# Kernel optimization log

Measured on AMD Instinct MI355X. Metric: run time of the kernel, lower is better.

## Reference

```python
import jax, jax.numpy as jnp
import numpy as np

B, S, H, V = 64, 512, 1024, 32000


def setup_inputs() -> dict:
    key = jax.random.key(0)
    ks = jax.random.split(key, 20)
    sd = 0.02
    inp = {
        'x': jax.random.randint(ks[0], (B, 1), 0, V),
        'h_prev': jax.random.normal(ks[1], (B, H), dtype=jnp.float32),
        'annotations': jax.random.normal(ks[2], (B, S, H), dtype=jnp.float32),
        # embedding table
        'emb': jax.random.normal(ks[3], (V, H), dtype=jnp.float32) * sd,
        # attention MLP: Linear(2H -> H), ReLU, Linear(H -> 1)
        'attn_W1': jax.random.normal(ks[4], (H, 2 * H), dtype=jnp.float32) * sd,
        'attn_b1': jnp.zeros((H,), jnp.float32),
        'attn_W2': jax.random.normal(ks[5], (1, H), dtype=jnp.float32) * sd,
        'attn_b2': jnp.zeros((1,), jnp.float32),
        # GRU cell linears (input_size = 2H). NOTE: original code has a bug where
        # weights_hr is never used (r uses weights_hz); we replicate that, so no Whr.
        'W_ir': jax.random.normal(ks[6], (H, 2 * H), dtype=jnp.float32) * sd,
        'b_ir': jnp.zeros((H,), jnp.float32),
        'W_iz': jax.random.normal(ks[7], (H, 2 * H), dtype=jnp.float32) * sd,
        'b_iz': jnp.zeros((H,), jnp.float32),
        'W_in': jax.random.normal(ks[8], (H, 2 * H), dtype=jnp.float32) * sd,
        'b_in': jnp.zeros((H,), jnp.float32),
        'W_hz': jax.random.normal(ks[9], (H, H), dtype=jnp.float32) * sd,
        'b_hz': jnp.zeros((H,), jnp.float32),
        'W_hn': jax.random.normal(ks[10], (H, H), dtype=jnp.float32) * sd,
        'b_hn': jnp.zeros((H,), jnp.float32),
        # output projection H -> V
        'W_out': jax.random.normal(ks[11], (V, H), dtype=jnp.float32) * sd,
        'b_out': jnp.zeros((V,), jnp.float32),
    }
    return inp


def _lin(x, W, b):
    # torch nn.Linear: y = x @ W.T + b, W has shape (out, in)
    return x @ W.T + b


def reference(x, h_prev, annotations, emb, attn_W1, attn_b1, attn_W2, attn_b2,
              W_ir, b_ir, W_iz, b_iz, W_in, b_in, W_hz, b_hz, W_hn, b_hn,
              W_out, b_out):
    # embedding lookup, squeeze time dim: (B, H)
    embed = emb[x[:, 0]]

    # additive attention: concat(annotations, expanded hidden) -> MLP -> softmax
    # split W1 over the concat axis to avoid materializing the [B,S,2H] concat:
    # concat @ W1.T == annotations @ W1[:, :H].T + hidden @ W1[:, H:].T
    hA = jnp.einsum('bsh,kh->bsk', annotations, attn_W1[:, :H])  # (B,S,H)
    hB = h_prev @ attn_W1[:, H:].T                               # (B,H)
    hidden_act = jax.nn.relu(hA + hB[:, None, :] + attn_b1)
    scores = jnp.einsum('bsk,k->bs', hidden_act, attn_W2[0]) + attn_b2[0]
    attention_weights = jax.nn.softmax(scores, axis=1)[:, :, None]  # (B,S,1)

    # context vector
    context = jnp.sum(attention_weights * annotations, axis=1)  # (B,H)
    xc = jnp.concatenate([context, embed], axis=1)              # (B,2H)

    # GRU cell (faithful to the original, including the weights_hz reuse in r)
    hz = _lin(h_prev, W_hz, b_hz)
    z = jax.nn.sigmoid(_lin(xc, W_iz, b_iz) + hz)
    r = jax.nn.sigmoid(_lin(xc, W_ir, b_ir) + hz)  # bug replicated: uses W_hz
    g = jnp.tanh(_lin(xc, W_in, b_in) + r * _lin(h_prev, W_hn, b_hn))
    h_new = (1.0 - z) * g + z * h_prev

    output = _lin(h_new, W_out, b_out)  # (B,V)
    return output, h_new, attention_weights
```

## Files before the change

### kernel.cpp

```cpp
#include <hip/hip_runtime.h>


typedef __bf16 bf16;
typedef __attribute__((ext_vector_type(4))) float  f32x4;
typedef __attribute__((ext_vector_type(4))) float  fx4;
typedef __attribute__((ext_vector_type(8))) bf16   bf16x8;
typedef __attribute__((ext_vector_type(4))) bf16   bf16x4;
typedef __attribute__((ext_vector_type(4))) unsigned int u32x4;
typedef __attribute__((ext_vector_type(2))) unsigned int u32x2;

#define MFMA16x16x32(a, b, c) __builtin_amdgcn_mfma_f32_16x16x32_bf16(a, b, c, 0, 0, 0)

#define Bb   64
#define Ss   512
#define Hh   1024
#define Vv   32000
#define Mtot (Bb * Ss)

#define WS_HNEW_B    131072
#define WS_XC_B      262144
#define WS_W1A_B     524288
#define WS_P_HB      2621440
#define WS_P_HZ      3670016
#define WS_P_HN      4718592
#define WS_P_IZ      5767168
#define WS_P_IR      6815744
#define WS_P_IN      7864320
#define WS_SCORES    8912896
#define WS_CTX       11010048
#define WS_ANNB      13107200

#define OUT_LOGITS   0
#define OUT_HNEW     2048000
#define OUT_AW       2113536

__device__ __forceinline__ float bf2f(unsigned short u) {
    unsigned int x = ((unsigned int)u) << 16;
    float f;
    __builtin_memcpy(&f, &x, 4);
    return f;
}

__device__ __forceinline__ void gload_lds16(const bf16* g, bf16* l)
{
    __builtin_amdgcn_global_load_lds(
        (const __attribute__((address_space(1))) unsigned int*)g,
        (__attribute__((address_space(3))) unsigned int*)l,
        16, 0, 0);
}

__global__ __launch_bounds__(256, 2) void k_pre(
    const int* __restrict__ x, const float* __restrict__ h_prev,
    const float* __restrict__ emb, const float* __restrict__ attn_W1,
    const float* __restrict__ W_hz, const float* __restrict__ W_hn,
    const float* __restrict__ ann,
    bf16* __restrict__ xc_b, bf16* __restrict__ W1a_b, bf16* __restrict__ annb,
    float* __restrict__ p_hB, float* __restrict__ p_hz, float* __restrict__ p_hn)
{
    __shared__ __align__(16) bf16 lA[2][64][72];
    __shared__ __align__(16) bf16 lB[2][64][72];

    int bid = blockIdx.x, t = threadIdx.x;

    if (bid >= 1280) {
        size_t i = ((size_t)(bid - 1280) * 256 + t) * 8;
        size_t stride = (size_t)2048 * 256 * 8;
        size_t n = (size_t)Mtot * Hh;
        for (; i < n; i += stride) {
            fx4 v0 = *(const fx4*)(ann + i);
            fx4 v1 = *(const fx4*)(ann + i + 4);
            bf16x8 o;
#pragma unroll
            for (int q = 0; q < 4; q++) { o[q] = (bf16)v0[q]; o[q + 4] = (bf16)v1[q]; }
            *(bf16x8*)(annb + i) = o;
        }
        return;
    }
    if (bid >= 192) {
        int sub = bid - 192;
        if (sub < 64) {
            int b = sub, row = x[b];
            for (int i = t; i < Hh; i += 256)
                xc_b[b * 2048 + Hh + i] = (bf16)emb[(size_t)row * Hh + i];
        } else {
            int row = sub - 64;
            int k4 = t * 4;
            fx4 v = *(const fx4*)(attn_W1 + (size_t)row * 2048 + k4);
            bf16x4 o;
#pragma unroll
            for (int q = 0; q < 4; q++) o[q] = (bf16)v[q];
            *(bf16x4*)(W1a_b + (size_t)row * Hh + k4) = o;
        }
        return;
    }

    int nb = bid & 15, sk = (bid >> 4) & 3, mat = bid >> 6;
    const float* Bp = (mat == 0) ? (attn_W1 + 1024) : (mat == 1 ? W_hz : W_hn);
    int ldb         = (mat == 0) ? 2048 : 1024;
    float* op       = (mat == 0) ? p_hB : (mat == 1 ? p_hz : p_hn);

    int n0 = nb * 64, k0 = sk * 256;
    int lane = t & 63, wid = t >> 6;
    int srow = t >> 2, schunk = t & 3;

    const float* agp = h_prev + (size_t)srow * 1024 + k0 + schunk * 16;
    const float* bgp = Bp + (size_t)(n0 + srow) * ldb + k0 + schunk * 16;

    f32x4 acc[4];
#pragma unroll
    for (int i = 0; i < 4; i++) acc[i] = (f32x4)0.0f;

    fx4 aRf[4], bRf[4];
#pragma unroll
    for (int q = 0; q < 4; q++) { aRf[q] = *(const fx4*)(agp + q * 4);
                                  bRf[q] = *(const fx4*)(bgp + q * 4); }
    {
        bf16x8 a0, a1, p0, p1;
#pragma unroll
        for (int q = 0; q < 4; q++) {
            a0[q] = (bf16)aRf[0][q]; a0[q + 4] = (bf16)aRf[1][q];
            a1[q] = (bf16)aRf[2][q]; a1[q + 4] = (bf16)aRf[3][q];
            p0[q] = (bf16)bRf[0][q]; p0[q + 4] = (bf16)bRf[1][q];
            p1[q] = (bf16)bRf[2][q]; p1[q + 4] = (bf16)bRf[3][q];
        }
        *(bf16x8*)&lA[0][srow][schunk * 16]     = a0;
        *(bf16x8*)&lA[0][srow][schunk * 16 + 8] = a1;
        *(bf16x8*)&lB[0][srow][schunk * 16]     = p0;
        *(bf16x8*)&lB[0][srow][schunk * 16 + 8] = p1;
    }
    __syncthreads();

    int cur = 0;
    for (int ks = 0; ks < 4; ks++) {
        if (ks + 1 < 4) {
#pragma unroll
            for (int q = 0; q < 4; q++) {
                aRf[q] = *(const fx4*)(agp + (ks + 1) * 64 + q * 4);
                bRf[q] = *(const fx4*)(bgp + (ks + 1) * 64 + q * 4);
            }
        }
        int rA = lane & 15;
        int kc = (lane >> 4) * 8;
#pragma unroll
        for (int kk = 0; kk < 2; kk++) {
            bf16x8 bfr = *(bf16x8*)&lB[cur][wid * 16 + rA][kk * 32 + kc];
#pragma unroll
            for (int i = 0; i < 4; i++) {
                bf16x8 af = *(bf16x8*)&lA[cur][i * 16 + rA][kk * 32 + kc];
                acc[i] = MFMA16x16x32(af, bfr, acc[i]);
            }
        }
        if (ks + 1 < 4) {
            int nxt = cur ^ 1;
            bf16x8 a0, a1, p0, p1;
#pragma unroll
            for (int q = 0; q < 4; q++) {
                a0[q] = (bf16)aRf[0][q]; a0[q + 4] = (bf16)aRf[1][q];
                a1[q] = (bf16)aRf[2][q]; a1[q + 4] = (bf16)aRf[3][q];
                p0[q] = (bf16)bRf[0][q]; p0[q + 4] = (bf16)bRf[1][q];
                p1[q] = (bf16)bRf[2][q]; p1[q + 4] = (bf16)bRf[3][q];
            }
            *(bf16x8*)&lA[nxt][srow][schunk * 16]     = a0;
            *(bf16x8*)&lA[nxt][srow][schunk * 16 + 8] = a1;
            *(bf16x8*)&lB[nxt][srow][schunk * 16]     = p0;
            *(bf16x8*)&lB[nxt][srow][schunk * 16 + 8] = p1;
        }
        __syncthreads();
        cur ^= 1;
    }

    int n = n0 + wid * 16 + (lane & 15);
#pragma unroll
    for (int i = 0; i < 4; i++)
#pragma unroll
        for (int r = 0; r < 4; r++) {
            int m = i * 16 + (lane >> 4) * 4 + r;
            op[(size_t)(sk * 64 + m) * 1024 + n] = acc[i][r];
        }
}

__global__ __launch_bounds__(256, 2) void k_sgemm(
    const bf16* __restrict__ A, int lda, int kchunk,
    const float* __restrict__ B0, const float* __restrict__ B1, const float* __restrict__ B2,
    int ldb0, int ldb1, int ldb2,
    float* __restrict__ o0, float* __restrict__ o1, float* __restrict__ o2,
    const float* __restrict__ bias, int N, int finalOut)
{
    __shared__ __align__(16) bf16 lA[2][64][72];
    __shared__ __align__(16) bf16 lB[2][64][72];

    int nb = blockIdx.x, sk = blockIdx.y, mat = blockIdx.z;
    const float* Bp = (mat == 0) ? B0 : (mat == 1 ? B1 : B2);
    int ldb         = (mat == 0) ? ldb0 : (mat == 1 ? ldb1 : ldb2);
    float* op       = (mat == 0) ? o0 : (mat == 1 ? o1 : o2);

    int n0 = nb * 64, k0 = sk * kchunk;
    int t = threadIdx.x, lane = t & 63, wid = t >> 6;
    int srow = t >> 2, schunk = t & 3;

    const bf16*  agp = A  + (size_t)srow * lda + k0 + schunk * 16;
    const float* bgp = Bp + (size_t)(n0 + srow) * ldb + k0 + schunk * 16;

    f32x4 acc[4];
#pragma unroll
    for (int i = 0; i < 4; i++) acc[i] = (f32x4)0.0f;

    u32x4 aR0, aR1; fx4 bRf[4];
    int nk = kchunk >> 6;

    aR0 = *(const u32x4*)(agp);
    aR1 = *(const u32x4*)(agp + 8);
#pragma unroll
    for (int q = 0; q < 4; q++) bRf[q] = *(const fx4*)(bgp + q * 4);
    {
        *(u32x4*)&lA[0][srow][schunk * 16]     = aR0;
        *(u32x4*)&lA[0][srow][schunk * 16 + 8] = aR1;
        bf16x8 p0, p1;
#pragma unroll
        for (int q = 0; q < 4; q++) {
            p0[q] = (bf16)bRf[0][q]; p0[q + 4] = (bf16)bRf[1][q];
            p1[q] = (bf16)bRf[2][q]; p1[q + 4] = (bf16)bRf[3][q];
        }
        *(bf16x8*)&lB[0][srow][schunk * 16]     = p0;
        *(bf16x8*)&lB[0][srow][schunk * 16 + 8] = p1;
    }
    __syncthreads();

    int cur = 0;
    for (int ks = 0; ks < nk; ks++) {
        if (ks + 1 < nk) {
            aR0 = *(const u32x4*)(agp + (ks + 1) * 64);
            aR1 = *(const u32x4*)(agp + (ks + 1) * 64 + 8);
#pragma unroll
            for (int q = 0; q < 4; q++) bRf[q] = *(const fx4*)(bgp + (ks + 1) * 64 + q * 4);
        }
        int rA = lane & 15;
        int kc = (lane >> 4) * 8;
#pragma unroll
        for (int kk = 0; kk < 2; kk++) {
            bf16x8 bfr = *(bf16x8*)&lB[cur][wid * 16 + rA][kk * 32 + kc];
#pragma unroll
            for (int i = 0; i < 4; i++) {
                bf16x8 af = *(bf16x8*)&lA[cur][i * 16 + rA][kk * 32 + kc];
                acc[i] = MFMA16x16x32(af, bfr, acc[i]);
            }
        }
        if (ks + 1 < nk) {
            int nxt = cur ^ 1;
            *(u32x4*)&lA[nxt][srow][schunk * 16]     = aR0;
            *(u32x4*)&lA[nxt][srow][schunk * 16 + 8] = aR1;
            bf16x8 p0, p1;
#pragma unroll
            for (int q = 0; q < 4; q++) {
                p0[q] = (bf16)bRf[0][q]; p0[q + 4] = (bf16)bRf[1][q];
                p1[q] = (bf16)bRf[2][q]; p1[q + 4] = (bf16)bRf[3][q];
            }
            *(bf16x8*)&lB[nxt][srow][schunk * 16]     = p0;
            *(bf16x8*)&lB[nxt][srow][schunk * 16 + 8] = p1;
        }
        __syncthreads();
        cur ^= 1;
    }

    int n = n0 + wid * 16 + (lane & 15);
#pragma unroll
    for (int i = 0; i < 4; i++) {
#pragma unroll
        for (int r = 0; r < 4; r++) {
            int m = i * 16 + (lane >> 4) * 4 + r;
            float v = acc[i][r];
            if (finalOut) op[(size_t)m * N + n] = v + bias[n];
            else          op[(size_t)(sk * 64 + m) * N + n] = v;
        }
    }
}

__global__ __launch_bounds__(512, 2) void k_attn(
    const bf16* __restrict__ annb, const bf16* __restrict__ Bw,
    const float* __restrict__ p_hB, const float* __restrict__ b1,
    const float* __restrict__ W2, float* __restrict__ scores_part)
{
    extern __shared__ char smem[];

    int bid = blockIdx.x;
    int wgid = (bid & 7) * 64 + (bid >> 3);
    int mb = wgid >> 2, nbp = wgid & 3;

    int t = threadIdx.x, lane = t & 63, wid = t >> 6;
    int wm = wid >> 2, wn = wid & 3;
    int r = lane & 15, q = lane >> 4;

    const bf16* aS = annb + (size_t)mb  * 262144
                   + (size_t)(wid * 32 + (lane >> 2)) * 1024 + (lane & 3) * 8;
    const bf16* bS = Bw   + (size_t)nbp * 262144
                   + (size_t)(wid * 32 + (lane >> 2)) * 1024 + (lane & 3) * 8;
    int sld = wid * 2048;

#define STAGE(kt) do { int bq_ = ((kt) & 3) * 32768;                         \
        const bf16* a_ = aS + (kt) * 32;                                     \
        const bf16* b_ = bS + (kt) * 32;                                     \
        gload_lds16(a_,         (bf16*)(smem + bq_ + sld));                  \
        gload_lds16(a_ + 16384, (bf16*)(smem + bq_ + sld + 1024));           \
        gload_lds16(b_,         (bf16*)(smem + bq_ + 16384 + sld));          \
        gload_lds16(b_ + 16384, (bf16*)(smem + bq_ + 16384 + sld + 1024));   \
    } while (0)

    int rAo[8], rBo[4];
#pragma unroll
    for (int i = 0; i < 8; i++)
        rAo[i] = (wm * 64 + (i & 3) * 16 + (i >> 2) * 128 + r) * 64 + q * 16;
#pragma unroll
    for (int j = 0; j < 4; j++)
        rBo[j] = 16384 + (wn * 32 + (j & 1) * 16 + (j >> 1) * 128 + r) * 64 + q * 16;

    f32x4 acc[8][4];
#pragma unroll
    for (int i = 0; i < 8; i++)
#pragma unroll
        for (int j = 0; j < 4; j++) acc[i][j] = (f32x4)0.0f;

    STAGE(0); STAGE(1); STAGE(2);
    asm volatile("s_waitcnt vmcnt(8)" ::: "memory");
    __builtin_amdgcn_s_barrier();

#pragma unroll 1
    for (int kt = 0; kt < 32; kt++) {
        const char* base = smem + (kt & 3) * 32768;
        bf16x8 aq[8], bq[4];
#pragma unroll
        for (int i = 0; i < 8; i++) aq[i] = *(const bf16x8*)(base + rAo[i]);
#pragma unroll
        for (int j = 0; j < 4; j++) bq[j] = *(const bf16x8*)(base + rBo[j]);
        if (kt < 29) STAGE(kt + 3);

        __builtin_amdgcn_s_setprio(1);
#pragma unroll
        for (int i = 0; i < 8; i++)
#pragma unroll
            for (int j = 0; j < 4; j++)
                acc[i][j] = MFMA16x16x32(aq[i], bq[j], acc[i][j]);
        __builtin_amdgcn_s_setprio(0);

        if (kt < 29)       { asm volatile("s_waitcnt vmcnt(8)" ::: "memory"); }
        else if (kt == 29) { asm volatile("s_waitcnt vmcnt(4)" ::: "memory"); }
        else if (kt == 30) { asm volatile("s_waitcnt vmcnt(0)" ::: "memory"); }
        if (kt < 31) __builtin_amdgcn_s_barrier();
    }
#undef STAGE

    int m0 = mb * 256, n0g = nbp * 256;
    int b = m0 >> 9;
    float hb[4], w2v[4];
#pragma unroll
    for (int j = 0; j < 4; j++) {
        int n = n0g + (j >> 1) * 128 + wn * 32 + (j & 1) * 16 + r;
        float h = p_hB[b * Hh + n] + p_hB[65536 + b * Hh + n]
                + p_hB[131072 + b * Hh + n] + p_hB[196608 + b * Hh + n];
        hb[j]  = h + b1[n];
        w2v[j] = W2[n];
    }
    float red[32];
#pragma unroll
    for (int i = 0; i < 8; i++)
#pragma unroll
        for (int rr = 0; rr < 4; rr++) {
            float s = 0.f;
#pragma unroll
            for (int j = 0; j < 4; j++) {
                float v = acc[i][j][rr] + hb[j];
                v = fmaxf(v, 0.f);
                s += v * w2v[j];
            }
            red[i * 4 + rr] = s;
        }
#pragma unroll
    for (int mask = 1; mask <= 8; mask <<= 1)
#pragma unroll
        for (int p = 0; p < 32; p++)
            red[p] += __shfl_xor(red[p], mask, 64);

    if (r == 0) {
        float* sp = scores_part + (size_t)(nbp * 4 + wn) * Mtot;
#pragma unroll
        for (int i = 0; i < 8; i++) {
            int m = m0 + wm * 64 + (i & 3) * 16 + (i >> 2) * 128 + q * 4;
#pragma unroll
            for (int rr = 0; rr < 4; rr++)
                sp[m + rr] = red[i * 4 + rr];
        }
    }
}

__global__ void k_softmax(const float* __restrict__ scores_part, float* __restrict__ aw)
{
    int b = blockIdx.x, s = threadIdx.x;
    int lane = s & 63, wid = s >> 6;
    float v = 0.f;
#pragma unroll
    for (int p = 0; p < 16; p++) v += scores_part[(size_t)p * Mtot + b * Ss + s];

    __shared__ float redm[8], redsum[8];
    float m = v;
#pragma unroll
    for (int mask = 32; mask; mask >>= 1) m = fmaxf(m, __shfl_xor(m, mask, 64));
    if (lane == 0) redm[wid] = m;
    __syncthreads();
    float bm = redm[0];
#pragma unroll
    for (int w = 1; w < 8; w++) bm = fmaxf(bm, redm[w]);

    float e = expf(v - bm);
    float ss = e;
#pragma unroll
    for (int mask = 32; mask; mask >>= 1) ss += __shfl_xor(ss, mask, 64);
    if (lane == 0) redsum[wid] = ss;
    __syncthreads();
    float tot = 0.f;
#pragma unroll
    for (int w = 0; w < 8; w++) tot += redsum[w];

    aw[b * Ss + s] = e / tot;
}

__global__ void k_context(const bf16* __restrict__ annb, const float* __restrict__ aw,
                          float* __restrict__ ctx_part)
{
    __shared__ float law[64];
    int bid = blockIdx.x;
    int b = bid >> 3, sc = bid & 7;
    int t = threadIdx.x;
    if (t < 64) law[t] = aw[b * Ss + sc * 64 + t];
    __syncthreads();
    int h0 = t * 4;
    const bf16* ap = annb + (size_t)(b * Ss + sc * 64) * Hh + h0;
    float a0 = 0, a1 = 0, a2 = 0, a3 = 0;
#pragma unroll 4
    for (int s2 = 0; s2 < 64; s2++) {
        float w = law[s2];
        u32x2 v = *(const u32x2*)(ap + (size_t)s2 * Hh);
        a0 += w * bf2f((unsigned short)(v[0] & 0xffff));
        a1 += w * bf2f((unsigned short)(v[0] >> 16));
        a2 += w * bf2f((unsigned short)(v[1] & 0xffff));
        a3 += w * bf2f((unsigned short)(v[1] >> 16));
    }
    fx4 o; o[0] = a0; o[1] = a1; o[2] = a2; o[3] = a3;
    *(fx4*)(ctx_part + sc * 65536 + b * Hh + h0) = o;
}

__global__ void k_xc(const float* __restrict__ ctx_part, bf16* __restrict__ xc_b)
{
    int idx = blockIdx.x * 256 + threadIdx.x;
    float c = 0.f;
#pragma unroll
    for (int p = 0; p < 8; p++) c += ctx_part[p * 65536 + idx];
    int b = idx >> 10, h = idx & 1023;
    xc_b[b * 2048 + h] = (bf16)c;
}

__global__ void k_gru(const float* __restrict__ p_iz, const float* __restrict__ p_ir,
                      const float* __restrict__ p_in, const float* __restrict__ p_hz,
                      const float* __restrict__ p_hn,
                      const float* __restrict__ b_iz, const float* __restrict__ b_ir,
                      const float* __restrict__ b_in, const float* __restrict__ b_hz,
                      const float* __restrict__ b_hn,
                      const float* __restrict__ h_prev,
                      float* __restrict__ out_h, bf16* __restrict__ h_new_b)
{
    int idx = blockIdx.x * 256 + threadIdx.x;
    int o = idx & 1023;
    float iz = p_iz[idx] + p_iz[65536 + idx] + p_iz[131072 + idx] + p_iz[196608 + idx];
    float ir = p_ir[idx] + p_ir[65536 + idx] + p_ir[131072 + idx] + p_ir[196608 + idx];
    float in_ = p_in[idx] + p_in[65536 + idx] + p_in[131072 + idx] + p_in[196608 + idx];
    float hz = p_hz[idx] + p_hz[65536 + idx] + p_hz[131072 + idx] + p_hz[196608 + idx];
    float hn = p_hn[idx] + p_hn[65536 + idx] + p_hn[131072 + idx] + p_hn[196608 + idx];
    hz += b_hz[o];
    hn += b_hn[o];
    float z = 1.f / (1.f + expf(-(iz + b_iz[o] + hz)));
    float r = 1.f / (1.f + expf(-(ir + b_ir[o] + hz)));
    float g = tanhf(in_ + b_in[o] + r * hn);
    float hp = h_prev[idx];
    float hnew = (1.f - z) * g + z * hp;
    out_h[idx] = hnew;
    h_new_b[idx] = (bf16)hnew;
}

extern "C" void kernel_launch(void* const* d_in, const int* in_sizes, int n_in,
                              void* d_out, int out_size, void* d_ws, size_t ws_size,
                              hipStream_t stream)
{
    const int*   x        = (const int*)d_in[0];
    const float* h_prev   = (const float*)d_in[1];
    const float* ann      = (const float*)d_in[2];
    const float* emb      = (const float*)d_in[3];
    const float* attn_W1  = (const float*)d_in[4];
    const float* attn_b1  = (const float*)d_in[5];
    const float* attn_W2  = (const float*)d_in[6];
    const float* W_ir     = (const float*)d_in[8];
    const float* b_ir     = (const float*)d_in[9];
    const float* W_iz     = (const float*)d_in[10];
    const float* b_iz     = (const float*)d_in[11];
    const float* W_in     = (const float*)d_in[12];
    const float* b_in     = (const float*)d_in[13];
    const float* W_hz     = (const float*)d_in[14];
    const float* b_hz     = (const float*)d_in[15];
    const float* W_hn     = (const float*)d_in[16];
    const float* b_hn     = (const float*)d_in[17];
    const float* W_out    = (const float*)d_in[18];
    const float* b_out    = (const float*)d_in[19];

    float* out = (float*)d_out;
    char*  ws  = (char*)d_ws;

    bf16*  h_new_b  = (bf16*)(ws + WS_HNEW_B);
    bf16*  xc_b     = (bf16*)(ws + WS_XC_B);
    bf16*  W1a_b    = (bf16*)(ws + WS_W1A_B);
    float* p_hB     = (float*)(ws + WS_P_HB);
    float* p_hz     = (float*)(ws + WS_P_HZ);
    float* p_hn     = (float*)(ws + WS_P_HN);
    float* p_iz     = (float*)(ws + WS_P_IZ);
    float* p_ir     = (float*)(ws + WS_P_IR);
    float* p_in     = (float*)(ws + WS_P_IN);
    float* scores_p = (float*)(ws + WS_SCORES);
    float* ctx_part = (float*)(ws + WS_CTX);
    bf16*  annb     = (bf16*)(ws + WS_ANNB);

    hipFuncSetAttribute(reinterpret_cast<const void*>(k_attn),
                        hipFuncAttributeMaxDynamicSharedMemorySize, 131072);

    k_pre<<<3328, 256, 0, stream>>>(x, h_prev, emb, attn_W1, W_hz, W_hn, ann,
                                    xc_b, W1a_b, annb, p_hB, p_hz, p_hn);

    k_attn<<<512, 512, 131072, stream>>>(annb, W1a_b, p_hB, attn_b1, attn_W2,
                                         scores_p);

    k_softmax<<<64, 512, 0, stream>>>(scores_p, out + OUT_AW);

    k_context<<<512, 256, 0, stream>>>(annb, out + OUT_AW, ctx_part);

    k_xc<<<256, 256, 0, stream>>>(ctx_part, xc_b);

    {
        dim3 g(16, 4, 3);
        k_sgemm<<<g, 256, 0, stream>>>(xc_b, 2048, 512,
                                       W_iz, W_ir, W_in, 2048, 2048, 2048,
                                       p_iz, p_ir, p_in, nullptr, 1024, 0);
    }

    k_gru<<<256, 256, 0, stream>>>(p_iz, p_ir, p_in, p_hz, p_hn,
                                   b_iz, b_ir, b_in, b_hz, b_hn,
                                   h_prev, out + OUT_HNEW, h_new_b);

    {
        dim3 g(500, 1, 1);
        k_sgemm<<<g, 256, 0, stream>>>(h_new_b, 1024, 1024,
                                       W_out, W_out, W_out, 1024, 1024, 1024,
                                       out + OUT_LOGITS, nullptr, nullptr,
                                       b_out, 32000, 1);
    }
}
```

Baseline: 169.2 us.

## Restructure attention GEMM main loop into 4-phase double-buffered K=64 schedule with swizzled LDS

After: 171.3 us. No clear change (+1.2%).

```diff
diff --git a/kernel.cpp b/kernel.cpp
--- a/kernel.cpp
+++ b/kernel.cpp
@@ -290,63 +290,95 @@
     int wm = wid >> 2, wn = wid & 3;
     int r = lane & 15, q = lane >> 4;
 
-    const bf16* aS = annb + (size_t)mb  * 262144
-                   + (size_t)(wid * 32 + (lane >> 2)) * 1024 + (lane & 3) * 8;
-    const bf16* bS = Bw   + (size_t)nbp * 262144
-                   + (size_t)(wid * 32 + (lane >> 2)) * 1024 + (lane & 3) * 8;
-    int sld = wid * 2048;
-
-#define STAGE(kt) do { int bq_ = ((kt) & 3) * 32768;                         \
-        const bf16* a_ = aS + (kt) * 32;                                     \
-        const bf16* b_ = bS + (kt) * 32;                                     \
-        gload_lds16(a_,         (bf16*)(smem + bq_ + sld));                  \
-        gload_lds16(a_ + 16384, (bf16*)(smem + bq_ + sld + 1024));           \
-        gload_lds16(b_,         (bf16*)(smem + bq_ + 16384 + sld));          \
-        gload_lds16(b_ + 16384, (bf16*)(smem + bq_ + 16384 + sld + 1024));   \
+    int srow = t >> 3;
+    int gc   = (t & 7) ^ (srow & 7);
+    size_t goff = (size_t)srow * 1024 + gc * 8;
+    int doff = wid * 1024;
+    const bf16* aSrc = annb + (size_t)mb * 262144;
+    const bf16* bSrc = Bw   + (size_t)nbp * 262144;
+
+    int e0 = (q ^ (r & 7)) * 16, e1 = e0 ^ 64;
+    int rowAoff = (wm * 64 + r) * 128;
+    int rowBoff = 32768 + (wn * 32 + r) * 128;
+
+#define STAGEOP(src, half, buf, mat, kt) do {                                  \
+        const bf16* s_ = (src) + (half) * 131072 + (size_t)(kt) * 64 + goff;   \
+        char* d_ = smem + (buf) * 65536 + (mat) * 32768 + (half) * 16384 + doff; \
+        gload_lds16(s_, (bf16*)d_);                                            \
+        gload_lds16(s_ + 65536, (bf16*)(d_ + 8192));                           \
     } while (0)
 
-    int rAo[8], rBo[4];
+#define VMW(n) asm volatile("s_waitcnt vmcnt(" #n ")" ::: "memory")
+
+    f32x4 acc[8][4];
 #pragma unroll
     for (int i = 0; i < 8; i++)
-        rAo[i] = (wm * 64 + (i & 3) * 16 + (i >> 2) * 128 + r) * 64 + q * 16;
-#pragma unroll
-    for (int j = 0; j < 4; j++)
-        rBo[j] = 16384 + (wn * 32 + (j & 1) * 16 + (j >> 1) * 128 + r) * 64 + q * 16;
-
-    f32x4 acc[8][4];
-#pragma unroll
-    for (int i = 0; i < 8; i++)
 #pragma unroll
         for (int j = 0; j < 4; j++) acc[i][j] = (f32x4)0.0f;
 
-    STAGE(0); STAGE(1); STAGE(2);
-    asm volatile("s_waitcnt vmcnt(8)" ::: "memory");
+    bf16x8 aq[4][2], bq[2][2];
+
+#define PHASE(IH, JH, RA, RB, STG, WAITQ) do {                                 \
+        if (RA) {                                                              \
+            _Pragma("unroll")                                                  \
+            for (int ip = 0; ip < 4; ip++) {                                   \
+                const char* pa_ = smem + cur * 65536 + (IH) * 16384            \
+                                + rowAoff + ip * 2048;                         \
+                aq[ip][0] = *(const bf16x8*)(pa_ + e0);                        \
+                aq[ip][1] = *(const bf16x8*)(pa_ + e1);                        \
+            }                                                                  \
+        }                                                                      \
+        if (RB) {                                                              \
+            _Pragma("unroll")                                                  \
+            for (int jp = 0; jp < 2; jp++) {                                   \
+                const char* pb_ = smem + cur * 65536 + (JH) * 16384            \
+                                + rowBoff + jp * 2048;                         \
+                bq[jp][0] = *(const bf16x8*)(pb_ + e0);                        \
+                bq[jp][1] = *(const bf16x8*)(pb_ + e1);                        \
+            }                                                                  \
+        }                                                                      \
+        STG;                                                                   \
+        __builtin_amdgcn_s_barrier();                                          \
+        __builtin_amdgcn_s_setprio(1);                                         \
+        _Pragma("unroll")                                                      \
+        for (int ip = 0; ip < 4; ip++)                                         \
+            _Pragma("unroll")                                                  \
+            for (int jp = 0; jp < 2; jp++)                                     \
+                _Pragma("unroll")                                              \
+                for (int ks = 0; ks < 2; ks++)                                 \
+                    acc[(IH) * 4 + ip][(JH) * 2 + jp] =                        \
+                        MFMA16x16x32(aq[ip][ks], bq[jp][ks],                   \
+                                     acc[(IH) * 4 + ip][(JH) * 2 + jp]);       \
+        __builtin_amdgcn_s_setprio(0);                                         \
+        WAITQ;                                                                 \
+        __builtin_amdgcn_s_barrier();                                          \
+    } while (0)
+
+    STAGEOP(aSrc, 0, 0, 0, 0);
+    STAGEOP(bSrc, 0, 0, 1, 0);
+    STAGEOP(aSrc, 1, 0, 0, 0);
+    STAGEOP(bSrc, 1, 0, 1, 0);
+    VMW(0);
     __builtin_amdgcn_s_barrier();
 
 #pragma unroll 1
-    for (int kt = 0; kt < 32; kt++) {
-        const char* base = smem + (kt & 3) * 32768;
-        bf16x8 aq[8], bq[4];
-#pragma unroll
-        for (int i = 0; i < 8; i++) aq[i] = *(const bf16x8*)(base + rAo[i]);
-#pragma unroll
-        for (int j = 0; j < 4; j++) bq[j] = *(const bf16x8*)(base + rBo[j]);
-        if (kt < 29) STAGE(kt + 3);
-
-        __builtin_amdgcn_s_setprio(1);
-#pragma unroll
-        for (int i = 0; i < 8; i++)
-#pragma unroll
-            for (int j = 0; j < 4; j++)
-                acc[i][j] = MFMA16x16x32(aq[i], bq[j], acc[i][j]);
-        __builtin_amdgcn_s_setprio(0);
-
-        if (kt < 29)       { asm volatile("s_waitcnt vmcnt(8)" ::: "memory"); }
-        else if (kt == 29) { asm volatile("s_waitcnt vmcnt(4)" ::: "memory"); }
-        else if (kt == 30) { asm volatile("s_waitcnt vmcnt(0)" ::: "memory"); }
-        if (kt < 31) __builtin_amdgcn_s_barrier();
-    }
-#undef STAGE
+    for (int kt = 0; kt < 15; kt++) {
+        int cur = kt & 1, nxt = cur ^ 1;
+        PHASE(0, 0, 1, 1, { STAGEOP(aSrc, 0, nxt, 0, kt + 1);
+                            STAGEOP(bSrc, 0, nxt, 1, kt + 1); }, VMW(6));
+        PHASE(1, 0, 1, 0, { STAGEOP(aSrc, 1, nxt, 0, kt + 1); }, VMW(6));
+        PHASE(1, 1, 0, 1, , (void)0);
+        PHASE(0, 1, 1, 0, { STAGEOP(bSrc, 1, nxt, 1, kt + 1); }, VMW(4));
+    }
+    {
+        int cur = 1;
+        PHASE(0, 0, 1, 1, , VMW(2));
+        PHASE(1, 0, 1, 0, , VMW(0));
+        PHASE(1, 1, 0, 1, , (void)0);
+        PHASE(0, 1, 1, 0, , (void)0);
+    }
+#undef PHASE
+#undef STAGEOP
 
     int m0 = mb * 256, n0g = nbp * 256;
     int b = m0 >> 9;
```
